# Optimization experiments

Measured on AMD Instinct MI355X. Metric: run time of the kernel, lower is better.

Reference implementation:

```python
import jax, jax.numpy as jnp
import numpy as np

MASK_ID = 103
TIMESTEPS = 200
B, T, V = 16, 512, 32000


def setup_inputs() -> dict:
    key = jax.random.key(0)
    k1, k2, k3, k4 = jax.random.split(key, 4)
    target_logits = jax.random.normal(k1, (B, T, V), dtype=jnp.float32)
    tokens = jax.random.randint(k2, (B, T), 0, V)
    gen_mask = jax.random.randint(k3, (B, T), 0, 2).astype(bool)
    # subset of generated positions are currently masked (as mid-loop state)
    is_masked = gen_mask & (jax.random.uniform(k4, (B, T)) < 0.6)
    target_ids = jnp.where(is_masked, MASK_ID, tokens)
    return {"target_logits": target_logits, "target_ids": target_ids,
            "gen_mask": gen_mask, "t": 100}


def _gamma_table():
    # cosine schedule: gamma = 1 - cos(pi/2 * s/T)^2, clamped to [0,1]
    steps = jnp.arange(TIMESTEPS + 1, dtype=jnp.float32)
    g = 1.0 - jnp.cos(jnp.pi / 2 * steps / TIMESTEPS) ** 2
    return jnp.clip(g, 0.0, 1.0)


def reference(target_logits, target_ids, gen_mask, t):
    """One reverse step of MaskDiffusion.p_sample_loop (t > 1 branch)."""
    gamma = _gamma_table()
    probs = jax.nn.softmax(target_logits, axis=-1)          # (B,T,V)
    pred_tokens = jnp.argmax(probs, axis=-1)                # (B,T)
    confidence = jnp.max(probs, axis=-1)                    # (B,T)

    gamma_prev = gamma[t - 1]
    n_gen = jnp.sum(gen_mask, axis=-1).astype(jnp.float32)  # (B,)
    n_mask_prev = jnp.maximum((gamma_prev * n_gen).astype(jnp.int32), 0)

    is_masked = target_ids == MASK_ID
    # positions not eligible for re-masking get +inf confidence
    conf_sort = jnp.where(gen_mask & is_masked, confidence, jnp.inf)
    sorted_idx = jnp.argsort(conf_sort, axis=-1)            # (B,T)

    # unmask everything that was masked, then re-mask the n_mask_prev
    # least-confident positions (vectorized rank-based scatter, no per-b loop)
    new_target = jnp.where(is_masked, pred_tokens, target_ids)
    ranks = jnp.arange(new_target.shape[1])[None, :]        # (1,T)
    remask_sorted = ranks < n_mask_prev[:, None]            # (B,T) in sorted order
    remask = jnp.zeros(new_target.shape, dtype=bool).at[
        jnp.arange(new_target.shape[0])[:, None], sorted_idx].set(remask_sorted)
    new_target = jnp.where(remask, MASK_ID, new_target)
    return new_target, confidence
```

## Files before the change

kernel.cpp:

```cpp
#include <hip/hip_runtime.h>
#include <hip/hip_bf16.h>
#include <math.h>

#define MASK_ID 103
#define NB 16
#define NT 512
#define NV 32000
#define BT (NB * NT)


__global__ void conf_kernel(const float* __restrict__ logits,
                            int* __restrict__ pred,
                            float* __restrict__ conf_f,
                            float* __restrict__ out_f) {
    const int row = blockIdx.x;
    const float4* p4 = (const float4*)(logits + (size_t)row * NV);
    const int tid = threadIdx.x;

    float m0 = -INFINITY, m1 = -INFINITY, m2 = -INFINITY, m3 = -INFINITY;
    int   i0 = 0, i1 = 0, i2 = 0, i3 = 0;
    float s0 = 0.f, s1 = 0.f, s2 = 0.f, s3 = 0.f;

    for (int j = tid; j < NV / 4; j += 256) {
        float4 v = p4[j];
        s0 += __expf(v.x);  if (v.x > m0) { m0 = v.x; i0 = 4 * j + 0; }
        s1 += __expf(v.y);  if (v.y > m1) { m1 = v.y; i1 = 4 * j + 1; }
        s2 += __expf(v.z);  if (v.z > m2) { m2 = v.z; i2 = 4 * j + 2; }
        s3 += __expf(v.w);  if (v.w > m3) { m3 = v.w; i3 = 4 * j + 3; }
    }

    float mm = m0; int ii = i0;
    if (m1 > mm || (m1 == mm && i1 < ii)) { mm = m1; ii = i1; }
    if (m2 > mm || (m2 == mm && i2 < ii)) { mm = m2; ii = i2; }
    if (m3 > mm || (m3 == mm && i3 < ii)) { mm = m3; ii = i3; }
    float ssum = (s0 + s1) + (s2 + s3);

    __shared__ float sm[256];
    __shared__ float ss[256];
    __shared__ int   si[256];
    sm[tid] = mm; ss[tid] = ssum; si[tid] = ii;
    __syncthreads();

    for (int off = 128; off > 0; off >>= 1) {
        if (tid < off) {
            float ma = sm[tid],       mb = sm[tid + off];
            int   ia = si[tid],       ib = si[tid + off];
            if (mb > ma || (mb == ma && ib < ia)) { sm[tid] = mb; si[tid] = ib; }
            ss[tid] = ss[tid] + ss[tid + off];
        }
        __syncthreads();
    }

    if (tid == 0) {
        float c = __expf(sm[0]) / ss[0];
        pred[row]       = si[0];
        conf_f[row]     = c;
        out_f[BT + row] = c;
    }
}

__global__ void remask_kernel(const int* __restrict__ ids,
                              const int* __restrict__ gmask,
                              const int* __restrict__ tptr,
                              const int* __restrict__ pred,
                              const float* __restrict__ conf,
                              float* __restrict__ out_f) {
    const int b   = blockIdx.x;
    const int tid = threadIdx.x;
    const int p0 = tid, p1 = tid + 256;
    const int off0 = b * NT + p0, off1 = b * NT + p1;

    __shared__ float cs[NT];
    __shared__ int   red[256];

    const int id0 = ids[off0], id1 = ids[off1];
    const int gm0 = gmask[off0], gm1 = gmask[off1];
    const bool mk0 = (id0 == MASK_ID), mk1 = (id1 == MASK_ID);
    cs[p0] = (gm0 && mk0) ? conf[off0] : INFINITY;
    cs[p1] = (gm1 && mk1) ? conf[off1] : INFINITY;
    red[tid] = (gm0 ? 1 : 0) + (gm1 ? 1 : 0);
    __syncthreads();

    for (int o = 128; o > 0; o >>= 1) {
        if (tid < o) red[tid] += red[tid + o];
        __syncthreads();
    }
    const int ngen = red[0];

    const int   tt = tptr[0];
    const float x  = (float)(M_PI / 2) * (float)(tt - 1) / 200.0f;
    const float cg = cosf(x);
    float g = 1.0f - cg * cg;
    g = fminf(fmaxf(g, 0.0f), 1.0f);
    int n_mask = (int)(g * (float)ngen);
    if (n_mask < 0) n_mask = 0;

    const float c0 = cs[p0], c1 = cs[p1];
    int r0 = 0, r1 = 0;
    for (int j = 0; j < NT; ++j) {
        float cj = cs[j];
        r0 += (cj < c0 || (cj == c0 && j < p0)) ? 1 : 0;
        r1 += (cj < c1 || (cj == c1 && j < p1)) ? 1 : 0;
    }

    int tk0 = mk0 ? pred[off0] : id0; if (r0 < n_mask) tk0 = MASK_ID;
    int tk1 = mk1 ? pred[off1] : id1; if (r1 < n_mask) tk1 = MASK_ID;
    out_f[off0] = (float)tk0;
    out_f[off1] = (float)tk1;
}


__global__ void fused_kernel(const float* __restrict__ logits,
                             const int* __restrict__ ids,
                             const int* __restrict__ gmask,
                             const int* __restrict__ tptr,
                             float* __restrict__ out_f) {
    const int b   = blockIdx.x;
    const int tid = threadIdx.x;

    __shared__ float rm[1024];
    __shared__ float rs[1024];
    __shared__ int   ri[1024];
    __shared__ float sconf[NT];
    __shared__ int   spred[NT];

    for (int t = 0; t < NT; ++t) {
        const int row = b * NT + t;
        const float4* p4 = (const float4*)(logits + (size_t)row * NV);
        float m = -INFINITY; float s = 0.0f; int idx = 0;
        for (int j = tid; j < NV / 4; j += 1024) {
            float4 v = p4[j];
            float vals[4] = {v.x, v.y, v.z, v.w};
            #pragma unroll
            for (int k = 0; k < 4; ++k) {
                float val = vals[k];
                s += __expf(val);
                if (val > m) { m = val; idx = 4 * j + k; }
            }
        }
        rm[tid] = m; rs[tid] = s; ri[tid] = idx;
        __syncthreads();
        for (int o = 512; o > 0; o >>= 1) {
            if (tid < o) {
                float ma = rm[tid],     mb = rm[tid + o];
                int   ia = ri[tid],     ib = ri[tid + o];
                if (mb > ma || (mb == ma && ib < ia)) { rm[tid] = mb; ri[tid] = ib; }
                rs[tid] = rs[tid] + rs[tid + o];
            }
            __syncthreads();
        }
        if (tid == 0) {
            float c = __expf(rm[0]) / rs[0];
            sconf[t] = c;
            spred[t] = ri[0];
            out_f[BT + row] = c;
        }
        __syncthreads();
    }

    ri[tid] = (tid < NT && gmask[b * NT + tid]) ? 1 : 0;
    __syncthreads();
    for (int o = 512; o > 0; o >>= 1) {
        if (tid < o) ri[tid] += ri[tid + o];
        __syncthreads();
    }
    const int ngen = ri[0];

    const int   tt = tptr[0];
    const float x  = (float)(M_PI / 2) * (float)(tt - 1) / 200.0f;
    const float cg = cosf(x);
    float g = 1.0f - cg * cg;
    g = fminf(fmaxf(g, 0.0f), 1.0f);
    int n_mask = (int)(g * (float)ngen);
    if (n_mask < 0) n_mask = 0;

    int id = 0; bool mk = false;
    if (tid < NT) {
        const int off = b * NT + tid;
        id = ids[off];
        const int gm = gmask[off];
        mk = (id == MASK_ID);
        rm[tid] = (gm && mk) ? sconf[tid] : INFINITY;
    }
    __syncthreads();
    if (tid < NT) {
        const int off = b * NT + tid;
        float ci = rm[tid];
        int rank = 0;
        for (int j = 0; j < NT; ++j) {
            float cj = rm[j];
            rank += (cj < ci || (cj == ci && j < tid)) ? 1 : 0;
        }
        int tk = mk ? spred[tid] : id;
        if (rank < n_mask) tk = MASK_ID;
        out_f[off] = (float)tk;
    }
}


extern "C" void kernel_launch(void* const* d_in, const int* in_sizes, int n_in,
                              void* d_out, int out_size, void* d_ws, size_t ws_size,
                              hipStream_t stream) {
    const float* logits = (const float*)d_in[0];
    const int*   ids    = (const int*)d_in[1];
    const int*   gmask  = (const int*)d_in[2];
    const int*   tptr   = (const int*)d_in[3];
    float* out = (float*)d_out;

    const size_t need = (size_t)BT * (sizeof(int) + sizeof(float));
    if (ws_size >= need && d_ws != nullptr) {
        int*   pred = (int*)d_ws;
        float* conf = (float*)((char*)d_ws + (size_t)BT * sizeof(int));
        conf_kernel<<<BT, 256, 0, stream>>>(logits, pred, conf, out);
        remask_kernel<<<NB, 256, 0, stream>>>(ids, gmask, tptr, pred, conf, out);
    } else {
        fused_kernel<<<NB, 1024, 0, stream>>>(logits, ids, gmask, tptr, out);
    }
}
```

Baseline: 206.3 us.

## Assign one wavefront per row in softmax-max kernel with shuffle reductions

The confidence kernel now maps each 64-lane wavefront to one vocabulary row, so each 256-thread block handles four rows. The shared-memory tree reduction and its block barriers are replaced by wave-level xor shuffles. The loop is unrolled to issue two float4 loads per iteration and keep eight independent accumulators for more memory-level parallelism. Each row is now read by fewer threads in a longer serial loop, which could lower latency hiding per row.

```diff
diff --git a/kernel.cpp b/kernel.cpp
--- a/kernel.cpp
+++ b/kernel.cpp
@@ -9,51 +9,64 @@
 #define BT (NB * NT)
 
 
-__global__ void conf_kernel(const float* __restrict__ logits,
-                            int* __restrict__ pred,
-                            float* __restrict__ conf_f,
-                            float* __restrict__ out_f) {
-    const int row = blockIdx.x;
+__global__ __launch_bounds__(256) void conf_kernel(const float* __restrict__ logits,
+                                                   int* __restrict__ pred,
+                                                   float* __restrict__ conf_f,
+                                                   float* __restrict__ out_f) {
+    const int wave = threadIdx.x >> 6;
+    const int lane = threadIdx.x & 63;
+    const int row  = blockIdx.x * 4 + wave;
     const float4* p4 = (const float4*)(logits + (size_t)row * NV);
-    const int tid = threadIdx.x;
-
-    float m0 = -INFINITY, m1 = -INFINITY, m2 = -INFINITY, m3 = -INFINITY;
-    int   i0 = 0, i1 = 0, i2 = 0, i3 = 0;
-    float s0 = 0.f, s1 = 0.f, s2 = 0.f, s3 = 0.f;
-
-    for (int j = tid; j < NV / 4; j += 256) {
-        float4 v = p4[j];
-        s0 += __expf(v.x);  if (v.x > m0) { m0 = v.x; i0 = 4 * j + 0; }
-        s1 += __expf(v.y);  if (v.y > m1) { m1 = v.y; i1 = 4 * j + 1; }
-        s2 += __expf(v.z);  if (v.z > m2) { m2 = v.z; i2 = 4 * j + 2; }
-        s3 += __expf(v.w);  if (v.w > m3) { m3 = v.w; i3 = 4 * j + 3; }
-    }
-
-    float mm = m0; int ii = i0;
-    if (m1 > mm || (m1 == mm && i1 < ii)) { mm = m1; ii = i1; }
-    if (m2 > mm || (m2 == mm && i2 < ii)) { mm = m2; ii = i2; }
-    if (m3 > mm || (m3 == mm && i3 < ii)) { mm = m3; ii = i3; }
-    float ssum = (s0 + s1) + (s2 + s3);
-
-    __shared__ float sm[256];
-    __shared__ float ss[256];
-    __shared__ int   si[256];
-    sm[tid] = mm; ss[tid] = ssum; si[tid] = ii;
-    __syncthreads();
-
-    for (int off = 128; off > 0; off >>= 1) {
-        if (tid < off) {
-            float ma = sm[tid],       mb = sm[tid + off];
-            int   ia = si[tid],       ib = si[tid + off];
-            if (mb > ma || (mb == ma && ib < ia)) { sm[tid] = mb; si[tid] = ib; }
-            ss[tid] = ss[tid] + ss[tid + off];
-        }
-        __syncthreads();
-    }
-
-    if (tid == 0) {
-        float c = __expf(sm[0]) / ss[0];
-        pred[row]       = si[0];
+
+    float m[8], s[8];
+    int   ix[8];
+    #pragma unroll
+    for (int k = 0; k < 8; ++k) { m[k] = -INFINITY; s[k] = 0.0f; ix[k] = 0; }
+
+    for (int j = 0; j < 62; ++j) {
+        const int ea = j * 512 + lane * 4;
+        const int eb = ea + 256;
+        float4 a = p4[ea >> 2];
+        float4 b = p4[eb >> 2];
+        float va[4] = {a.x, a.y, a.z, a.w};
+        float vb[4] = {b.x, b.y, b.z, b.w};
+        #pragma unroll
+        for (int k = 0; k < 4; ++k) {
+            s[k] += __expf(va[k]);
+            if (va[k] > m[k]) { m[k] = va[k]; ix[k] = ea + k; }
+            s[k + 4] += __expf(vb[k]);
+            if (vb[k] > m[k + 4]) { m[k + 4] = vb[k]; ix[k + 4] = eb + k; }
+        }
+    }
+    {
+        const int et = 62 * 512 + lane * 4;
+        float4 a = p4[et >> 2];
+        float va[4] = {a.x, a.y, a.z, a.w};
+        #pragma unroll
+        for (int k = 0; k < 4; ++k) {
+            s[k] += __expf(va[k]);
+            if (va[k] > m[k]) { m[k] = va[k]; ix[k] = et + k; }
+        }
+    }
+
+    float mm = m[0]; int ii = ix[0];
+    #pragma unroll
+    for (int k = 1; k < 8; ++k)
+        if (m[k] > mm || (m[k] == mm && ix[k] < ii)) { mm = m[k]; ii = ix[k]; }
+    float ssum = ((s[0] + s[1]) + (s[2] + s[3])) + ((s[4] + s[5]) + (s[6] + s[7]));
+
+    #pragma unroll
+    for (int off = 32; off > 0; off >>= 1) {
+        float mb = __shfl_xor(mm, off);
+        int   ib = __shfl_xor(ii, off);
+        float sb = __shfl_xor(ssum, off);
+        if (mb > mm || (mb == mm && ib < ii)) { mm = mb; ii = ib; }
+        ssum += sb;
+    }
+
+    if (lane == 0) {
+        float c = __expf(mm) / ssum;
+        pred[row]       = ii;
         conf_f[row]     = c;
         out_f[BT + row] = c;
     }
@@ -211,7 +224,7 @@
     if (ws_size >= need && d_ws != nullptr) {
         int*   pred = (int*)d_ws;
         float* conf = (float*)((char*)d_ws + (size_t)BT * sizeof(int));
-        conf_kernel<<<BT, 256, 0, stream>>>(logits, pred, conf, out);
+        conf_kernel<<<BT / 4, 256, 0, stream>>>(logits, pred, conf, out);
         remask_kernel<<<NB, 256, 0, stream>>>(ids, gmask, tptr, pred, conf, out);
     } else {
         fused_kernel<<<NB, 1024, 0, stream>>>(logits, ids, gmask, tptr, out);
```

Result: slower. 212.1 us (+2.8%).
